# Kernel tuning notes

Hardware: AMD Instinct MI355X
Metric: run time of the kernel (lower is better)

Reference implementation:

```python
import jax, jax.numpy as jnp
import numpy as np

B = 2
D = 256
NH = 8
DH = D // NH
L = 4
K = 2                       # sampling grid per box side
NP = K * K                  # sampled points per level
FF = 1024
NQ = 300
NE = 6
ND = 6
REF_SIZE = 4.0
SHAPES = ((64, 64), (32, 32), (16, 16), (8, 8))
S = sum(h * w for h, w in SHAPES)


def make_ref_windows():
    ws = []
    for (H, W) in SHAPES:
        y = (jnp.arange(1, H + 1, dtype=jnp.float32) - 0.5) / (H + 1e-6)
        x = (jnp.arange(1, W + 1, dtype=jnp.float32) - 0.5) / (W + 1e-6)
        yy, xx = jnp.meshgrid(y, x, indexing='ij')
        ctr = jnp.stack([xx, yy], -1).reshape(-1, 2)
        size = jnp.broadcast_to(jnp.array([REF_SIZE / W, REF_SIZE / H], jnp.float32), ctr.shape)
        ws.append(jnp.concatenate([ctr, size], -1))
    return jnp.broadcast_to(jnp.concatenate(ws, 0)[None], (B, S, 4))


def layernorm(x, g, b):
    m = jnp.mean(x, -1, keepdims=True)
    v = jnp.mean((x - m) ** 2, -1, keepdims=True)
    return (x - m) / jnp.sqrt(v + 1e-5) * g + b


def inverse_sigmoid(x, eps=1e-5):
    x = jnp.clip(x, eps, 1.0 - eps)
    return jnp.log(x / (1.0 - x))


def bilinear_sample(vl, pts, Hl, Wl):
    # vl: [B, Hl*Wl, NH, DH], pts: [B, N, NP, 2] normalized to [0,1]
    x = pts[..., 0] * Wl - 0.5
    y = pts[..., 1] * Hl - 0.5
    x0f = jnp.floor(x); y0f = jnp.floor(y)
    wx = x - x0f; wy = y - y0f
    x0 = x0f.astype(jnp.int32); y0 = y0f.astype(jnp.int32)
    Bn, N, P = x.shape

    def gather(yi, xi):
        valid = ((xi >= 0) & (xi < Wl) & (yi >= 0) & (yi < Hl)).astype(vl.dtype)
        idx = jnp.clip(yi, 0, Hl - 1) * Wl + jnp.clip(xi, 0, Wl - 1)
        g = jnp.take_along_axis(vl, idx.reshape(Bn, N * P, 1, 1), axis=1)
        return g.reshape(Bn, N, P, NH, DH) * valid[..., None, None]

    w00 = ((1 - wx) * (1 - wy))[..., None, None]
    w01 = (wx * (1 - wy))[..., None, None]
    w10 = ((1 - wx) * wy)[..., None, None]
    w11 = (wx * wy)[..., None, None]
    return (gather(y0, x0) * w00 + gather(y0, x0 + 1) * w01
            + gather(y0 + 1, x0) * w10 + gather(y0 + 1, x0 + 1) * w11)


def box_attention(q, memory, ref_windows, Wv, bv, Wa, ba, Wo, bo):
    # q: [B,N,D], memory: [B,S,D], ref_windows: [B,N,4] (cx,cy,w,h)
    Bn, N, _ = q.shape
    v = (memory @ Wv + bv).reshape(Bn, memory.shape[1], NH, DH)
    attn = jax.nn.softmax((q @ Wa + ba).reshape(Bn, N, NH, L * NP), axis=-1)
    g = (jnp.arange(K, dtype=jnp.float32) + 0.5) / K - 0.5   # grid fractions in box
    gy, gx = jnp.meshgrid(g, g, indexing='ij')
    grid = jnp.stack([gx.ravel(), gy.ravel()], -1)           # [NP,2]
    pts = ref_windows[:, :, None, :2] + grid[None, None] * ref_windows[:, :, None, 2:]
    out = jnp.zeros((Bn, N, NH, DH), q.dtype)
    start = 0
    for l, (Hl, Wl) in enumerate(SHAPES):
        sl = Hl * Wl
        sampled = bilinear_sample(v[:, start:start + sl], pts, Hl, Wl)  # [B,N,NP,NH,DH]
        out = out + jnp.einsum('bnphd,bnhp->bnhd', sampled, attn[..., l * NP:(l + 1) * NP])
        start += sl
    return out.reshape(Bn, N, D) @ Wo + bo


def mha(q_in, k_in, v_in, Wqkv, bqkv, Wo, bo):
    Bn, N, _ = q_in.shape
    q = (q_in @ Wqkv[:, :D] + bqkv[:D]).reshape(Bn, N, NH, DH)
    k = (k_in @ Wqkv[:, D:2 * D] + bqkv[D:2 * D]).reshape(Bn, N, NH, DH)
    v = (v_in @ Wqkv[:, 2 * D:] + bqkv[2 * D:]).reshape(Bn, N, NH, DH)
    a = jax.nn.softmax(jnp.einsum('bqhd,bkhd->bhqk', q, k) / jnp.sqrt(jnp.float32(DH)), axis=-1)
    o = jnp.einsum('bhqk,bkhd->bqhd', a, v).reshape(Bn, N, D)
    return o @ Wo + bo


def pos_embed_2d(coords):
    # coords: [B,N,2] -> [B,N,D] sine embedding (deformable-DETR style)
    npf = D // 2
    dim_t = 10000.0 ** (2.0 * (jnp.arange(npf) // 2) / npf)
    p = coords[..., None] * (2 * np.pi) / dim_t               # [B,N,2,npf]
    p = jnp.stack([jnp.sin(p[..., 0::2]), jnp.cos(p[..., 1::2])], -1)
    return p.reshape(coords.shape[0], coords.shape[1], 2 * npf)


def reference(src, pos, eWv, ebv, eWa, eba, eWo, ebo, eW1, eb1, eW2, eb2,
              en1g, en1b, en2g, en2b,
              dWqkv, dbqkv, dWso, dbso, dWv, dbv, dWa, dba, dWo, dbo,
              dW1, db1, dW2, db2, dn1g, dn1b, dn2g, dn2b, dn3g, dn3b,
              cls_w, cls_b, bb_w1, bb_b1, bb_w2, bb_b2, bb_w3, bb_b3,
              el_w, el_b, el_g, el_beta):
    ref_windows = make_ref_windows()
    out = src
    for i in range(NE):
        a = box_attention(out + pos, out, ref_windows, eWv[i], ebv[i], eWa[i], eba[i], eWo[i], ebo[i])
        out = layernorm(out + a, en1g[i], en1b[i])
        f = jax.nn.relu(out @ eW1[i] + eb1[i]) @ eW2[i] + eb2[i]
        out = layernorm(out + f, en2g[i], en2b[i])
    # proposal selection (topk + gather)
    valid = jnp.all((ref_windows[..., :2] > 0.01) & (ref_windows[..., :2] < 0.99), axis=-1)
    logits = (out @ cls_w + cls_b)[..., 0]
    logits = jnp.where(valid, logits, -65504.0)
    _, idx = jax.lax.top_k(logits, NQ)
    q_emb = jnp.take_along_axis(out, idx[..., None], axis=1)
    tgt = layernorm(jax.lax.stop_gradient(q_emb) @ el_w + el_b, el_g, el_beta)
    ref_sel = jnp.take_along_axis(ref_windows, idx[..., None], axis=1)
    h = jax.nn.relu(q_emb @ bb_w1 + bb_b1)
    h = jax.nn.relu(h @ bb_w2 + bb_b2)
    tmp = h @ bb_w3 + bb_b3 + inverse_sigmoid(ref_sel)
    out_ref = jax.lax.stop_gradient(jax.nn.sigmoid(tmp))
    query_pos = pos_embed_2d(out_ref[..., :2]) + pos_embed_2d(out_ref[..., 2:])
    # decoder
    x = tgt
    inter = []
    for i in range(ND):
        qk = x + query_pos
        sa = mha(qk, qk, x, dWqkv[i], dbqkv[i], dWso[i], dbso[i])
        x = layernorm(x + sa, dn1g[i], dn1b[i])
        ca = box_attention(x + query_pos, out, out_ref, dWv[i], dbv[i], dWa[i], dba[i], dWo[i], dbo[i])
        x = layernorm(x + ca, dn2g[i], dn2b[i])
        f = jax.nn.relu(x @ dW1[i] + db1[i]) @ dW2[i] + db2[i]
        x = layernorm(x + f, dn3g[i], dn3b[i])
        inter.append(x)
    return jnp.stack(inter)  # [ND, B, NQ, D]


def setup_inputs() -> dict:
    key = jax.random.key(0)
    kit = iter(jax.random.split(key, 80))
    def rn(shape, s=0.02):
        return jax.random.normal(next(kit), shape, jnp.float32) * s
    z = lambda *sh: jnp.zeros(sh, jnp.float32)
    o = lambda *sh: jnp.ones(sh, jnp.float32)
    A = NH * L * NP
    return dict(
        src=jax.random.normal(next(kit), (B, S, D), jnp.float32),
        pos=jax.random.normal(next(kit), (B, S, D), jnp.float32),
        eWv=rn((NE, D, D)), ebv=z(NE, D), eWa=rn((NE, D, A)), eba=z(NE, A),
        eWo=rn((NE, D, D)), ebo=z(NE, D),
        eW1=rn((NE, D, FF)), eb1=z(NE, FF), eW2=rn((NE, FF, D)), eb2=z(NE, D),
        en1g=o(NE, D), en1b=z(NE, D), en2g=o(NE, D), en2b=z(NE, D),
        dWqkv=rn((ND, D, 3 * D)), dbqkv=z(ND, 3 * D),
        dWso=rn((ND, D, D)), dbso=z(ND, D),
        dWv=rn((ND, D, D)), dbv=z(ND, D), dWa=rn((ND, D, A)), dba=z(ND, A),
        dWo=rn((ND, D, D)), dbo=z(ND, D),
        dW1=rn((ND, D, FF)), db1=z(ND, FF), dW2=rn((ND, FF, D)), db2=z(ND, D),
        dn1g=o(ND, D), dn1b=z(ND, D), dn2g=o(ND, D), dn2b=z(ND, D), dn3g=o(ND, D), dn3b=z(ND, D),
        cls_w=rn((D, 1)), cls_b=z(1),
        bb_w1=rn((D, D)), bb_b1=z(D), bb_w2=rn((D, D)), bb_b2=z(D),
        bb_w3=rn((D, 4)), bb_b3=z(4),
        el_w=rn((D, D)), el_b=z(D), el_g=o(D), el_beta=z(D),
    )
```

## Files before the change

kernel.cpp:

```cpp
#include <hip/hip_runtime.h>
#include <hip/hip_bf16.h>
#include <math.h>

typedef unsigned short u16;
typedef unsigned int u32;
typedef unsigned long long u64;

#define Bc   2
#define NHc  8
#define Sc   5440
#define NQc  300
#define NEc  6
#define NDc  6
#define FFc  1024
#define BSc  (Bc*Sc)
#define BNQc (Bc*NQc)

__device__ __forceinline__ float us2f(u16 u) {
    union { float f; unsigned v; } x; x.v = ((unsigned)u) << 16; return x.f;
}

__device__ __forceinline__ u16 f2bf(float f) {
    unsigned u = __float_as_uint(f);
    unsigned r = u + 0x7FFFu + ((u >> 16) & 1u);
    return (u16)(r >> 16);
}
__device__ __forceinline__ float bf2f(u16 u) { return us2f(u); }
__device__ __forceinline__ unsigned pk2(u16 a, u16 b) { return (unsigned)a | ((unsigned)b << 16); }

__device__ __forceinline__ int xcd_swz(int orig, int nwg) {
    int xcd = orig & 7;
    int q = nwg >> 3, r = nwg & 7;
    int base = (xcd < r) ? xcd * (q + 1) : r * (q + 1) + (xcd - r) * q;
    return base + (orig >> 3);
}

using bf16x8 = __attribute__((ext_vector_type(8))) short;
using f32x4  = __attribute__((ext_vector_type(4))) float;

__global__ void k_detect(const u16* __restrict__ src, int* __restrict__ flag) {
    __shared__ int cnt;
    if (threadIdx.x == 0) cnt = 0;
    __syncthreads();
    u16 v = src[threadIdx.x];
    int e = (v >> 7) & 0xFF;
    int plaus = (e == 0) || (e >= 107 && e <= 131);
    atomicAdd(&cnt, plaus);
    __syncthreads();
    if (threadIdx.x == 0) *flag = (cnt >= 224) ? 1 : 0;
}

struct CvtArgs {
    const void* in[48];
    long off[48];
    int n[48];
    int cnt;
    long total;
};
__global__ void k_cvt_all8(CvtArgs args, float* __restrict__ out,
                           const int* __restrict__ flag) {
    long g = ((long)blockIdx.x * 256 + threadIdx.x) * 8;
    if (g >= args.total) return;
    int lo = 0, hi = args.cnt - 1;
    while (lo < hi) {
        int mid = (lo + hi + 1) >> 1;
        if (args.off[mid] <= g) lo = mid; else hi = mid - 1;
    }
    long local = g - args.off[lo];
    long n = (long)args.n[lo];
    float v[8];
#pragma unroll
    for (int j = 0; j < 8; ++j) v[j] = 0.f;
    if (*flag) {
        const u16* p = (const u16*)args.in[lo] + local;
        if (local + 8 <= n) {
            uint4 r = *(const uint4*)p;
            const u16* pu = (const u16*)&r;
#pragma unroll
            for (int j = 0; j < 8; ++j) v[j] = us2f(pu[j]);
        } else {
            for (int j = 0; j < 8; ++j)
                if (local + j < n) v[j] = us2f(p[j]);
        }
    } else {
        const float* p = (const float*)args.in[lo] + local;
        if (local + 8 <= n) {
            float4 a = ((const float4*)p)[0];
            float4 b = ((const float4*)p)[1];
            v[0] = a.x; v[1] = a.y; v[2] = a.z; v[3] = a.w;
            v[4] = b.x; v[5] = b.y; v[6] = b.z; v[7] = b.w;
        } else {
            for (int j = 0; j < 8; ++j)
                if (local + j < n) v[j] = p[j];
        }
    }
    float4 o0, o1;
    o0.x = v[0]; o0.y = v[1]; o0.z = v[2]; o0.w = v[3];
    o1.x = v[4]; o1.y = v[5]; o1.z = v[6]; o1.w = v[7];
    ((float4*)(out + g))[0] = o0;
    ((float4*)(out + g))[1] = o1;
}

__global__ void k_addf2(const float* __restrict__ a, const float* __restrict__ pos,
                        u16* __restrict__ ah, u16* __restrict__ al,
                        u16* __restrict__ ph, u16* __restrict__ pl, int n) {
    int i = blockIdx.x * 256 + threadIdx.x;
    if (i >= n) return;
    float x = a[i];
    u16 h = f2bf(x);
    ah[i] = h;
    al[i] = f2bf(x - bf2f(h));
    float s = x + pos[i];
    u16 h2 = f2bf(s);
    ph[i] = h2;
    pl[i] = f2bf(s - bf2f(h2));
}

template<int RELU>
__global__ __launch_bounds__(256) void k_mgemm(
    const u16* __restrict__ Ah, const u16* __restrict__ Al,
    const float* __restrict__ W, const u16* __restrict__ Wraw, int ldw,
    const float* __restrict__ bias,
    float* __restrict__ C, u16* __restrict__ Ch, u16* __restrict__ Cl,
    int ldc, int K,
    const int* __restrict__ flag) {
    __shared__ __align__(16) u16 lsAH[4096];
    __shared__ __align__(16) u16 lsAL[4096];
    __shared__ __align__(16) u16 lsBH[4096];
    __shared__ __align__(16) u16 lsBL[4096];
    const int t = threadIdx.x;
    int lin = blockIdx.x + gridDim.x * blockIdx.y;
    lin = xcd_swz(lin, gridDim.x * gridDim.y);
    const int row0 = (lin / gridDim.x) * 128, col0 = (lin % gridDim.x) * 128;
    const int fast = *flag;

    const int c0 = t, c1 = 256 + t;
    const u16* a0h = Ah + (size_t)(row0 + (c0 & 127)) * K + (c0 >> 7) * 8;
    const u16* a1h = Ah + (size_t)(row0 + (c1 & 127)) * K + (c1 >> 7) * 8;
    const u16* a0l = Al + (size_t)(row0 + (c0 & 127)) * K + (c0 >> 7) * 8;
    const u16* a1l = Al + (size_t)(row0 + (c1 & 127)) * K + (c1 >> 7) * 8;

    const int bkp = t >> 4, bno = t & 15;
    const float* bp = W + (size_t)(bkp * 2) * ldw + col0 + bno * 8;
    const u16*  brp = Wraw + (size_t)(bkp * 2) * ldw + col0 + bno * 8;

    const int lane = t & 63;
    const int w = t >> 6;
    const int wr = (w >> 1) * 64, wc = (w & 1) * 64;
    const int kg = lane >> 4, lr = lane & 15;

    f32x4 acc[4][4] = {};
    uint4 aU0h, aU1h, aU0l, aU1l;
    float4 bR[4];
    uint4 bU0, bU1;
    aU0h = *(const uint4*)a0h;
    aU1h = *(const uint4*)a1h;
    aU0l = *(const uint4*)a0l;
    aU1l = *(const uint4*)a1l;
    if (fast) {
        bU0 = *(const uint4*)brp;
        bU1 = *(const uint4*)(brp + ldw);
    } else {
        const float4* q0 = (const float4*)bp;
        const float4* q1 = (const float4*)(bp + ldw);
        bR[0] = q0[0]; bR[1] = q0[1]; bR[2] = q1[0]; bR[3] = q1[1];
    }

    for (int k0 = 0; k0 < K; k0 += 32) {
        if (k0) __syncthreads();
        *(uint4*)&lsAH[(unsigned)c0 * 8u] = aU0h;
        *(uint4*)&lsAH[(unsigned)c1 * 8u] = aU1h;
        *(uint4*)&lsAL[(unsigned)c0 * 8u] = aU0l;
        *(uint4*)&lsAL[(unsigned)c1 * 8u] = aU1l;
        {
            unsigned bb = (unsigned)(bkp >> 2) * 1024u + (unsigned)(bkp & 3) * 2u;
            if (fast) {
                const u16* e0 = (const u16*)&bU0;
                const u16* e1 = (const u16*)&bU1;
#pragma unroll
                for (int j = 0; j < 8; ++j) {
                    int slot = bno * 8 + (j ^ (bno & 7));
                    *(unsigned*)&lsBH[bb + (unsigned)slot * 8u] = pk2(e0[j], e1[j]);
                }
            } else {
                float e0f[8], e1f[8];
                *(float4*)&e0f[0] = bR[0]; *(float4*)&e0f[4] = bR[1];
                *(float4*)&e1f[0] = bR[2]; *(float4*)&e1f[4] = bR[3];
#pragma unroll
                for (int j = 0; j < 8; ++j) {
                    int slot = bno * 8 + (j ^ (bno & 7));
                    u16 h0 = f2bf(e0f[j]), h1 = f2bf(e1f[j]);
                    *(unsigned*)&lsBH[bb + (unsigned)slot * 8u] = pk2(h0, h1);
                    u16 l0 = f2bf(e0f[j] - bf2f(h0));
                    u16 l1 = f2bf(e1f[j] - bf2f(h1));
                    *(unsigned*)&lsBL[bb + (unsigned)slot * 8u] = pk2(l0, l1);
                }
            }
        }
        __syncthreads();
        if (k0 + 32 < K) {
            aU0h = *(const uint4*)(a0h + k0 + 32);
            aU1h = *(const uint4*)(a1h + k0 + 32);
            aU0l = *(const uint4*)(a0l + k0 + 32);
            aU1l = *(const uint4*)(a1l + k0 + 32);
            if (fast) {
                bU0 = *(const uint4*)(brp + (size_t)(k0 + 32) * ldw);
                bU1 = *(const uint4*)(brp + (size_t)(k0 + 33) * ldw);
            } else {
                const float4* q0 = (const float4*)(bp + (size_t)(k0 + 32) * ldw);
                const float4* q1 = (const float4*)(bp + (size_t)(k0 + 33) * ldw);
                bR[0] = q0[0]; bR[1] = q0[1]; bR[2] = q1[0]; bR[3] = q1[1];
            }
        }
        bf16x8 aH[4], aL[4], bH[4], bL[4];
#pragma unroll
        for (int mi = 0; mi < 4; ++mi) {
            unsigned ia = (unsigned)kg * 1024u + (unsigned)(wr + mi * 16 + lr) * 8u;
            aH[mi] = *(const bf16x8*)&lsAH[ia];
            aL[mi] = *(const bf16x8*)&lsAL[ia];
        }
#pragma unroll
        for (int ni = 0; ni < 4; ++ni) {
            int c = wc + ni * 16 + lr;
            int slot = (c & ~7) | ((c ^ (c >> 3)) & 7);
            unsigned ib = (unsigned)kg * 1024u + (unsigned)slot * 8u;
            bH[ni] = *(const bf16x8*)&lsBH[ib];
            if (!fast) bL[ni] = *(const bf16x8*)&lsBL[ib];
        }
#pragma unroll
        for (int mi = 0; mi < 4; ++mi)
#pragma unroll
            for (int ni = 0; ni < 4; ++ni) {
                acc[mi][ni] = __builtin_amdgcn_mfma_f32_16x16x32_bf16(aH[mi], bH[ni], acc[mi][ni], 0, 0, 0);
                acc[mi][ni] = __builtin_amdgcn_mfma_f32_16x16x32_bf16(aL[mi], bH[ni], acc[mi][ni], 0, 0, 0);
            }
        if (!fast) {
#pragma unroll
            for (int mi = 0; mi < 4; ++mi)
#pragma unroll
                for (int ni = 0; ni < 4; ++ni)
                    acc[mi][ni] = __builtin_amdgcn_mfma_f32_16x16x32_bf16(aH[mi], bL[ni], acc[mi][ni], 0, 0, 0);
        }
    }
    const int rb = row0 + wr + (lane >> 4) * 4;
#pragma unroll
    for (int ni = 0; ni < 4; ++ni) {
        int cc = col0 + wc + ni * 16 + lr;
        float bv = bias[cc];
#pragma unroll
        for (int mi = 0; mi < 4; ++mi) {
#pragma unroll
            for (int r2 = 0; r2 < 4; ++r2) {
                int rr = rb + mi * 16 + r2;
                float v = acc[mi][ni][r2] + bv;
                if (RELU) v = fmaxf(v, 0.f);
                size_t ox = (size_t)rr * ldc + cc;
                if (C) C[ox] = v;
                if (Ch) {
                    u16 h = f2bf(v);
                    Ch[ox] = h;
                    Cl[ox] = f2bf(v - bf2f(h));
                }
            }
        }
    }
}

template<int RELU>
__global__ __launch_bounds__(256) void k_dgemm(
    const float* __restrict__ A, int lda,
    const float* __restrict__ W, int ldw, int wcol0,
    const float* __restrict__ bias,
    float* __restrict__ C, int ldc,
    int M, int N, int K) {
    __shared__ float As[2][16][68];
    __shared__ float Bs[2][16][68];
    int t = threadIdx.x;
    int row0 = blockIdx.y * 64, col0 = blockIdx.x * 64;
    int ti = t >> 4, tj = t & 15;
    int arow = t >> 2, akq = (t & 3) << 2;
    int bk = t >> 4, bn = (t & 15) << 2;
    bool aok = (row0 + arow) < M;
    const float* ap = A + (size_t)(row0 + arow) * lda + akq;
    const float* bp = W + (size_t)bk * ldw + wcol0 + col0 + bn;
    float4 aR = aok ? *(const float4*)ap : make_float4(0.f, 0.f, 0.f, 0.f);
    float4 bR = *(const float4*)bp;
    As[0][akq + 0][arow] = aR.x;
    As[0][akq + 1][arow] = aR.y;
    As[0][akq + 2][arow] = aR.z;
    As[0][akq + 3][arow] = aR.w;
    *(float4*)&Bs[0][bk][bn] = bR;
    __syncthreads();
    int cur = 0;
    float acc[4][4] = {};
    for (int k0 = 0; k0 < K; k0 += 16) {
        bool more = (k0 + 16) < K;
        if (more) {
            aR = aok ? *(const float4*)(ap + k0 + 16) : make_float4(0.f, 0.f, 0.f, 0.f);
            bR = *(const float4*)(bp + (size_t)(k0 + 16) * ldw);
        }
#pragma unroll
        for (int k = 0; k < 16; ++k) {
            float a[4], b[4];
#pragma unroll
            for (int r = 0; r < 4; ++r) a[r] = As[cur][k][ti * 4 + r];
#pragma unroll
            for (int c = 0; c < 4; ++c) b[c] = Bs[cur][k][tj * 4 + c];
#pragma unroll
            for (int r = 0; r < 4; ++r)
#pragma unroll
                for (int c = 0; c < 4; ++c) acc[r][c] += a[r] * b[c];
        }
        if (more) {
            int nxt = cur ^ 1;
            As[nxt][akq + 0][arow] = aR.x;
            As[nxt][akq + 1][arow] = aR.y;
            As[nxt][akq + 2][arow] = aR.z;
            As[nxt][akq + 3][arow] = aR.w;
            *(float4*)&Bs[nxt][bk][bn] = bR;
            __syncthreads();
            cur = nxt;
        }
    }
    for (int r = 0; r < 4; ++r) {
        int rr = row0 + ti * 4 + r;
        if (rr >= M) continue;
        for (int c = 0; c < 4; ++c) {
            int cc = col0 + tj * 4 + c;
            float v = acc[r][c] + bias[cc];
            if (RELU) v = fmaxf(v, 0.f);
            C[(size_t)rr * ldc + cc] = v;
        }
    }
}

__global__ __launch_bounds__(256) void k_gemm4(
    const float* __restrict__ A, const float* __restrict__ W,
    const float* __restrict__ bias, const float* __restrict__ rsel,
    float* __restrict__ oref, int M, int K) {
    int row = blockIdx.x * 64 + (threadIdx.x >> 2);
    int col = threadIdx.x & 3;
    if (row >= M) return;
    float acc = 0.f;
    const float* a = A + (size_t)row * K;
    for (int k = 0; k < K; ++k) acc += a[k] * W[k * 4 + col];
    float tmp = acc + bias[col];
    float r = rsel[(size_t)row * 4 + col];
    r = fminf(fmaxf(r, 1e-5f), 1.f - 1e-5f);
    float v = tmp + logf(r / (1.f - r));
    oref[(size_t)row * 4 + col] = 1.f / (1.f + __expf(-v));
}

__global__ void k_ln(const float* __restrict__ a, const float* __restrict__ b,
                     const float* __restrict__ g, const float* __restrict__ be,
                     float* __restrict__ o,
                     u16* __restrict__ oh, u16* __restrict__ ol,
                     const float* __restrict__ padd, float* __restrict__ opadd,
                     u16* __restrict__ oph, u16* __restrict__ opl,
                     void* __restrict__ sdst, size_t soff,
                     const int* __restrict__ flag) {
    int row = blockIdx.x;
    int t = threadIdx.x;
    __shared__ float red[256];
    size_t ix = (size_t)row * 256 + t;
    float x = a[ix];
    if (b) x += b[ix];
    red[t] = x;
    __syncthreads();
    for (int s = 128; s > 0; s >>= 1) { if (t < s) red[t] += red[t + s]; __syncthreads(); }
    float mean = red[0] / 256.f;
    __syncthreads();
    float d = x - mean;
    red[t] = d * d;
    __syncthreads();
    for (int s = 128; s > 0; s >>= 1) { if (t < s) red[t] += red[t + s]; __syncthreads(); }
    float var = red[0] / 256.f;
    float y = d * rsqrtf(var + 1e-5f) * g[t] + be[t];
    o[ix] = y;
    if (oh) {
        u16 h = f2bf(y);
        oh[ix] = h;
        ol[ix] = f2bf(y - bf2f(h));
    }
    if (padd) {
        float z = y + padd[ix];
        if (opadd) opadd[ix] = z;
        if (oph) {
            u16 h = f2bf(z);
            oph[ix] = h;
            opl[ix] = f2bf(z - bf2f(h));
        }
    }
    if (sdst) {
        if (*flag) ((__hip_bfloat16*)sdst)[soff + ix] = __float2bfloat16(y);
        else       ((float*)sdst)[soff + ix] = y;
    }
}

__global__ void k_refw(float* __restrict__ rw) {
    int s = blockIdx.x * 256 + threadIdx.x;
    if (s >= Sc) return;
    int start, HW;
    if (s < 4096)      { start = 0;    HW = 64; }
    else if (s < 5120) { start = 4096; HW = 32; }
    else if (s < 5376) { start = 5120; HW = 16; }
    else               { start = 5376; HW = 8;  }
    int loc = s - start;
    int i = loc / HW, j = loc % HW;
    rw[s * 4 + 0] = (j + 0.5f) / ((float)HW + 1e-6f);
    rw[s * 4 + 1] = (i + 0.5f) / ((float)HW + 1e-6f);
    rw[s * 4 + 2] = 4.0f / (float)HW;
    rw[s * 4 + 3] = 4.0f / (float)HW;
}

__global__ __launch_bounds__(256) void k_box_sample4(
    const float* __restrict__ v, const float* __restrict__ attn,
    const float* __restrict__ refw, int ref_bs,
    float* __restrict__ out, u16* __restrict__ outh, u16* __restrict__ outl,
    int N) {
    const int t = threadIdx.x;
    const int qi = t >> 6, lane = t & 63;
    const int blk = xcd_swz(blockIdx.x, gridDim.x);
    const int n = blk * 4 + qi;
    const int b = blockIdx.y;
    if (n >= N) return;
    const float* arow = attn + ((size_t)b * N + n) * 128;
    float2 wl = *(const float2*)(arow + lane * 2);
    float m = fmaxf(wl.x, wl.y);
#pragma unroll
    for (int d2 = 1; d2 < 8; d2 <<= 1) m = fmaxf(m, __shfl_xor(m, d2, 8));
    float e0 = __expf(wl.x - m), e1 = __expf(wl.y - m);
    float s = e0 + e1;
#pragma unroll
    for (int d2 = 1; d2 < 8; d2 <<= 1) s += __shfl_xor(s, d2, 8);
    float inv = 1.f / s;
    e0 *= inv; e1 *= inv;

    const float* rw = refw + (size_t)ref_bs * b + (size_t)n * 4;
    float cx = rw[0], cy = rw[1], bw = rw[2], bh = rw[3];
    const float* vb = v + (size_t)b * Sc * 256 + lane * 4;
    float4 acc = make_float4(0.f, 0.f, 0.f, 0.f);
    int start = 0;
    const int HWs[4] = {64, 32, 16, 8};
#pragma unroll
    for (int l = 0; l < 4; ++l) {
        int HW = HWs[l];
#pragma unroll
        for (int p = 0; p < 4; ++p) {
            float gx = (p & 1) ? 0.25f : -0.25f;
            float gy = (p >> 1) ? 0.25f : -0.25f;
            float x = (cx + gx * bw) * (float)HW - 0.5f;
            float y = (cy + gy * bh) * (float)HW - 0.5f;
            float x0f = floorf(x), y0f = floorf(y);
            float wx = x - x0f, wy = y - y0f;
            int x0 = (int)x0f, y0 = (int)y0f;
            float4 smp = make_float4(0.f, 0.f, 0.f, 0.f);
            if (x0 >= 0 && x0 < HW && y0 >= 0 && y0 < HW) {
                float4 g4 = *(const float4*)(vb + (size_t)(start + y0 * HW + x0) * 256);
                float wgt = (1.f - wx) * (1.f - wy);
                smp.x += wgt * g4.x; smp.y += wgt * g4.y; smp.z += wgt * g4.z; smp.w += wgt * g4.w;
            }
            if (x0 + 1 >= 0 && x0 + 1 < HW && y0 >= 0 && y0 < HW) {
                float4 g4 = *(const float4*)(vb + (size_t)(start + y0 * HW + x0 + 1) * 256);
                float wgt = wx * (1.f - wy);
                smp.x += wgt * g4.x; smp.y += wgt * g4.y; smp.z += wgt * g4.z; smp.w += wgt * g4.w;
            }
            if (x0 >= 0 && x0 < HW && y0 + 1 >= 0 && y0 + 1 < HW) {
                float4 g4 = *(const float4*)(vb + (size_t)(start + (y0 + 1) * HW + x0) * 256);
                float wgt = (1.f - wx) * wy;
                smp.x += wgt * g4.x; smp.y += wgt * g4.y; smp.z += wgt * g4.z; smp.w += wgt * g4.w;
            }
            if (x0 + 1 >= 0 && x0 + 1 < HW && y0 + 1 >= 0 && y0 + 1 < HW) {
                float4 g4 = *(const float4*)(vb + (size_t)(start + (y0 + 1) * HW + x0 + 1) * 256);
                float wgt = wx * wy;
                smp.x += wgt * g4.x; smp.y += wgt * g4.y; smp.z += wgt * g4.z; smp.w += wgt * g4.w;
            }
            const int idx = l * 4 + p;
            float wsel = (idx & 1) ? e1 : e0;
            float wv = __shfl(wsel, (lane & ~7) | (idx >> 1), 64);
            acc.x += wv * smp.x; acc.y += wv * smp.y;
            acc.z += wv * smp.z; acc.w += wv * smp.w;
        }
        start += HW * HW;
    }
    size_t obase = ((size_t)b * N + n) * 256 + lane * 4;
    if (out) *(float4*)(out + obase) = acc;
    if (outh) {
        ushort4 h, lo;
        h.x = f2bf(acc.x); h.y = f2bf(acc.y); h.z = f2bf(acc.z); h.w = f2bf(acc.w);
        lo.x = f2bf(acc.x - bf2f(h.x)); lo.y = f2bf(acc.y - bf2f(h.y));
        lo.z = f2bf(acc.z - bf2f(h.z)); lo.w = f2bf(acc.w - bf2f(h.w));
        *(ushort4*)(outh + obase) = h;
        *(ushort4*)(outl + obase) = lo;
    }
}

__global__ void k_cls(const float* __restrict__ x, const float* __restrict__ w,
                      const float* __restrict__ cb, const float* __restrict__ rw,
                      float* __restrict__ logits) {
    int row = blockIdx.x;
    int t = threadIdx.x;
    __shared__ float red[256];
    red[t] = x[(size_t)row * 256 + t] * w[t];
    __syncthreads();
    for (int s = 128; s > 0; s >>= 1) { if (t < s) red[t] += red[t + s]; __syncthreads(); }
    if (t == 0) {
        int s = row % Sc;
        float cx = rw[s * 4], cy = rw[s * 4 + 1];
        bool valid = (cx > 0.01f) && (cx < 0.99f) && (cy > 0.01f) && (cy < 0.99f);
        logits[row] = valid ? (red[0] + cb[0]) : -65504.0f;
    }
}

__global__ void k_topk(const float* __restrict__ logits, int* __restrict__ idxout) {
    int b = blockIdx.x;
    int t = threadIdx.x;
    __shared__ unsigned keys[Sc];
    __shared__ int hist[256];
    __shared__ int suf[257];
    __shared__ unsigned sprefix;
    __shared__ int sR;
    __shared__ int cnt;
    __shared__ u64 cand[512];
    for (int i = t; i < Sc; i += 256) {
        union { float f; unsigned u; } x;
        x.f = logits[(size_t)b * Sc + i];
        unsigned u = x.u;
        keys[i] = (u & 0x80000000u) ? ~u : (u | 0x80000000u);
    }
    if (t == 0) { sprefix = 0; sR = NQc; suf[256] = 0; }
    __syncthreads();
    for (int shift = 24; shift >= 0; shift -= 8) {
        hist[t] = 0;
        __syncthreads();
        unsigned pref = sprefix;
        int R = sR;
        unsigned pmask = (shift == 24) ? 0u : (0xFFFFFFFFu << (shift + 8));
        for (int i = t; i < Sc; i += 256) {
            unsigned kk = keys[i];
            if ((kk & pmask) == (pref & pmask))
                atomicAdd(&hist[(kk >> shift) & 255], 1);
        }
        __syncthreads();
        suf[t] = hist[t];
        __syncthreads();
        for (int s2 = 1; s2 < 256; s2 <<= 1) {
            int vv = suf[t] + ((t + s2 < 256) ? suf[t + s2] : 0);
            __syncthreads();
            suf[t] = vv;
            __syncthreads();
        }
        if (suf[t] >= R && suf[t + 1] < R) {
            sR = R - suf[t + 1];
            sprefix = pref | ((unsigned)t << shift);
        }
        __syncthreads();
    }
    unsigned T = sprefix;
    if (t == 0) cnt = 0;
    __syncthreads();
    for (int i = t; i < Sc; i += 256) {
        unsigned kk = keys[i];
        if (kk >= T) {
            int slot = atomicAdd(&cnt, 1);
            if (slot < 512)
                cand[slot] = ~((((u64)kk) << 32) | (u64)(0xFFFFFFFFu - (unsigned)i));
        }
    }
    __syncthreads();
    int total = cnt < 512 ? cnt : 512;
    for (int i = t; i < 512; i += 256)
        if (i >= total) cand[i] = 0xFFFFFFFFFFFFFFFFull;
    __syncthreads();
    for (int i = t; i < 512; i += 256) {
        if (i >= total) continue;
        u64 mine = cand[i];
        int rank = 0;
        for (int j = 0; j < 512; ++j) rank += (cand[j] < mine) ? 1 : 0;
        if (rank < NQc) {
            u64 c = ~mine;
            idxout[b * NQc + rank] = (int)(0xFFFFFFFFu - (unsigned)(c & 0xFFFFFFFFull));
        }
    }
}

__global__ void k_gather(const float* __restrict__ x, const float* __restrict__ rw,
                         const int* __restrict__ idx, float* __restrict__ qemb,
                         float* __restrict__ refsel) {
    int q = blockIdx.x, b = blockIdx.y;
    int t = threadIdx.x;
    int id = idx[b * NQc + q];
    qemb[((size_t)b * NQc + q) * 256 + t] = x[((size_t)b * Sc + id) * 256 + t];
    if (t < 4) refsel[((size_t)b * NQc + q) * 4 + t] = rw[id * 4 + t];
}

__global__ void k_qpos(const float* __restrict__ outref, float* __restrict__ qpos) {
    int n = blockIdx.x, b = blockIdx.y;
    int t = threadIdx.x;
    const float* orf = outref + ((size_t)b * NQc + n) * 4;
    int c = t >> 7;
    int j = (t & 127) >> 1;
    int si = t & 1;
    float tj = powf(10000.f, (float)j / 64.f);
    float sc = 6.283185307179586f / tj;
    float v1 = orf[c] * sc;
    float v2 = orf[2 + c] * sc;
    float r = si ? (cosf(v1) + cosf(v2)) : (sinf(v1) + sinf(v2));
    qpos[((size_t)b * NQc + n) * 256 + t] = r;
}

#define NSPL 10
#define SPLW 30
__global__ __launch_bounds__(256) void k_mha2(
    const float* __restrict__ qk, const float* __restrict__ v,
    float* __restrict__ opart, float* __restrict__ mlpart) {
    __shared__ float lsK[SPLW][256];
    __shared__ float lsV[SPLW][256];
    const int t = threadIdx.x;
    const int h = t >> 5, ql = t & 31;
    const int b = blockIdx.y, z = blockIdx.z;
    const int n = blockIdx.x * 32 + ql;
    const bool qok = n < NQc;
    const int kstart = z * SPLW;
    for (int f = t; f < SPLW * 64; f += 256) {
        int r = f >> 6, c4 = f & 63;
        int krow = kstart + r;
        float4 kv = *(const float4*)(qk + (size_t)(b * NQc + krow) * 512 + 256 + c4 * 4);
        float4 vv = *(const float4*)(v + (size_t)(b * NQc + krow) * 256 + c4 * 4);
        *(float4*)&lsK[r][c4 * 4] = kv;
        *(float4*)&lsV[r][c4 * 4] = vv;
    }
    __syncthreads();
    float q[32];
    {
        const float* qp = qk + (size_t)(b * NQc + (qok ? n : 0)) * 512 + h * 32;
#pragma unroll
        for (int j4 = 0; j4 < 8; ++j4) {
            float4 f = ((const float4*)qp)[j4];
            q[j4 * 4 + 0] = f.x; q[j4 * 4 + 1] = f.y;
            q[j4 * 4 + 2] = f.z; q[j4 * 4 + 3] = f.w;
        }
    }
    const float scale = 0.17677669529663688f;
    float s[SPLW];
#pragma unroll
    for (int kk = 0; kk < SPLW; ++kk) {
        float acc = 0.f;
        const float* kr = &lsK[kk][h * 32];
#pragma unroll
        for (int j4 = 0; j4 < 8; ++j4) {
            float4 kf = ((const float4*)kr)[j4];
            acc += q[j4*4+0]*kf.x + q[j4*4+1]*kf.y + q[j4*4+2]*kf.z + q[j4*4+3]*kf.w;
        }
        s[kk] = acc * scale;
    }
    float m = s[0];
#pragma unroll
    for (int kk = 1; kk < SPLW; ++kk) m = fmaxf(m, s[kk]);
    float o[32];
#pragma unroll
    for (int j = 0; j < 32; ++j) o[j] = 0.f;
    float l = 0.f;
#pragma unroll
    for (int kk = 0; kk < SPLW; ++kk) {
        float e = __expf(s[kk] - m);
        l += e;
        const float* vr = &lsV[kk][h * 32];
#pragma unroll
        for (int j4 = 0; j4 < 8; ++j4) {
            float4 vf = ((const float4*)vr)[j4];
            o[j4*4+0] += e * vf.x; o[j4*4+1] += e * vf.y;
            o[j4*4+2] += e * vf.z; o[j4*4+3] += e * vf.w;
        }
    }
    if (qok) {
        float* op = opart + ((size_t)z * BNQc + (size_t)b * NQc + n) * 256 + h * 32;
#pragma unroll
        for (int j4 = 0; j4 < 8; ++j4) {
            float4 f;
            f.x = o[j4*4+0]; f.y = o[j4*4+1]; f.z = o[j4*4+2]; f.w = o[j4*4+3];
            ((float4*)op)[j4] = f;
        }
        float* mlp = mlpart + ((size_t)z * BNQc + (size_t)b * NQc + n) * 16 + h * 2;
        mlp[0] = m; mlp[1] = l;
    }
}

__global__ void k_mha_comb(const float* __restrict__ opart, const float* __restrict__ mlpart,
                           float* __restrict__ out) {
    int row = blockIdx.x;
    int t = threadIdx.x;
    int h = t >> 5;
    float mm[NSPL], ll[NSPL];
    float M = -3.0e38f;
#pragma unroll
    for (int z = 0; z < NSPL; ++z) {
        mm[z] = mlpart[((size_t)z * BNQc + row) * 16 + h * 2];
        ll[z] = mlpart[((size_t)z * BNQc + row) * 16 + h * 2 + 1];
        M = fmaxf(M, mm[z]);
    }
    float denom = 0.f, osum = 0.f;
#pragma unroll
    for (int z = 0; z < NSPL; ++z) {
        float a = __expf(mm[z] - M);
        denom += ll[z] * a;
        osum += opart[((size_t)z * BNQc + row) * 256 + t] * a;
    }
    out[(size_t)row * 256 + t] = osum / denom;
}

extern "C" void kernel_launch(void* const* d_in, const int* in_sizes, int n_in,
                              void* d_out, int out_size, void* d_ws, size_t ws_size,
                              hipStream_t stream) {
    char* base = (char*)d_ws;
    size_t off = 0;
    auto allocB = [&](size_t bytes) {
        char* p = base + off;
        off = (off + bytes + 255) & ~(size_t)255;
        return p;
    };
    int* flag = (int*)allocB(16);
    auto allocF = [&](size_t n) { return (float*)allocB(n * 4); };
    auto allocH = [&](size_t n) { return (u16*)allocB(n * 2); };

    k_detect<<<1, 256, 0, stream>>>((const u16*)d_in[0], flag);

    CvtArgs ca;
    long acc = 0;
    int ninp = n_in < 48 ? n_in : 48;
    for (int i = 0; i < 48; ++i) {
        int idx2 = i < ninp ? i : ninp - 1;
        ca.in[i] = d_in[idx2];
        ca.n[i] = (i < ninp) ? in_sizes[i] : 0;
        ca.off[i] = acc;
        acc += ((long)ca.n[i] + 63) & ~63L;
    }
    ca.cnt = 48;
    ca.total = acc;
    float* cvtbase = allocF((size_t)acc);
    k_cvt_all8<<<(int)((acc / 8 + 255) / 256), 256, 0, stream>>>(ca, cvtbase, flag);
    float* F[48];
    for (int i = 0; i < 48; ++i) F[i] = cvtbase + ca.off[i];

    const size_t BSD = (size_t)BSc * 256;
    float* enc    = F[0];
    u16* encH  = allocH(BSD);  u16* encL  = allocH(BSD);
    u16* pbufH = allocH(BSD);  u16* pbufL = allocH(BSD);
    u16* tbufH = allocH(BSD);  u16* tbufL = allocH(BSD);
    u16* ffnhH = allocH((size_t)BSc * FFc);
    u16* ffnhL = allocH((size_t)BSc * FFc);
    float* vbuf   = allocF(BSD);
    float* gout   = allocF(BSD);
    float* attnb  = allocF((size_t)BSc * 128);
    float* refw   = allocF(Sc * 4);
    float* logit  = allocF(BSc);
    int*   idx    = (int*)allocB(BNQc * 4);
    float* qemb   = allocF((size_t)BNQc * 256);
    float* rsel   = allocF(BNQc * 4);
    float* xbuf   = allocF((size_t)BNQc * 256);
    float* qposb  = allocF((size_t)BNQc * 256);
    float* dqk    = allocF((size_t)BNQc * 256);
    float* dqk512 = allocF((size_t)BNQc * 512);
    float* dv     = allocF((size_t)BNQc * 256);
    float* dt1    = allocF((size_t)BNQc * 256);
    float* dt2    = allocF((size_t)BNQc * 256);
    float* datt   = allocF((size_t)BNQc * 128);
    float* dffnh  = allocF((size_t)BNQc * FFc);
    float* h1f    = allocF((size_t)BNQc * 256);
    float* h2f    = allocF((size_t)BNQc * 256);
    float* oref   = allocF(BNQc * 4);
    float* opart  = allocF((size_t)NSPL * BNQc * 256);
    float* mlpart = allocF((size_t)NSPL * BNQc * 16);
    (void)ws_size; (void)out_size;

    auto MG = [&](int relu, const u16* Ah, const u16* Al, int widx, size_t woff, int ldw,
                  const float* bias, float* Cf, u16* Ch, u16* Cl, int ldc, int N, int K) {
        const float* Wf = F[widx] + woff;
        const u16* Wraw = (const u16*)d_in[widx] + woff;
        dim3 g(N / 128, BSc / 128);
        if (relu) k_mgemm<1><<<g, 256, 0, stream>>>(Ah, Al, Wf, Wraw, ldw, bias, Cf, Ch, Cl, ldc, K, flag);
        else      k_mgemm<0><<<g, 256, 0, stream>>>(Ah, Al, Wf, Wraw, ldw, bias, Cf, Ch, Cl, ldc, K, flag);
    };
    auto DG = [&](int relu, const float* A, int lda, const float* W, int ldw, int wcol0,
                  const float* bias, float* C, int ldc, int M, int N, int K) {
        dim3 g(N / 64, (M + 63) / 64);
        if (relu) k_dgemm<1><<<g, 256, 0, stream>>>(A, lda, W, ldw, wcol0, bias, C, ldc, M, N, K);
        else      k_dgemm<0><<<g, 256, 0, stream>>>(A, lda, W, ldw, wcol0, bias, C, ldc, M, N, K);
    };

    const int nBSD = (int)BSD;
    k_refw<<<(Sc + 255) / 256, 256, 0, stream>>>(refw);
    k_addf2<<<(nBSD + 255) / 256, 256, 0, stream>>>(enc, F[1], encH, encL, pbufH, pbufL, nBSD);

    for (int i = 0; i < NEc; ++i) {
        MG(0, encH, encL, 2, (size_t)i * 65536, 256, F[3] + i * 256, vbuf, nullptr, nullptr, 256, 256, 256);
        MG(0, pbufH, pbufL, 4, (size_t)i * 32768, 128, F[5] + i * 128, attnb, nullptr, nullptr, 128, 128, 256);
        k_box_sample4<<<dim3((Sc + 3) / 4, Bc), 256, 0, stream>>>(vbuf, attnb, refw, 0,
                                                                  nullptr, tbufH, tbufL, Sc);
        MG(0, tbufH, tbufL, 6, (size_t)i * 65536, 256, F[7] + i * 256, gout, nullptr, nullptr, 256, 256, 256);
        k_ln<<<BSc, 256, 0, stream>>>(enc, gout, F[12] + i * 256, F[13] + i * 256,
                                      enc, encH, encL,
                                      nullptr, nullptr, nullptr, nullptr,
                                      nullptr, 0, flag);
        MG(1, encH, encL, 8, (size_t)i * 262144, 1024, F[9] + i * 1024,
           nullptr, ffnhH, ffnhL, 1024, 1024, 256);
        MG(0, ffnhH, ffnhL, 10, (size_t)i * 262144, 256, F[11] + i * 256,
           gout, nullptr, nullptr, 256, 256, 1024);
        k_ln<<<BSc, 256, 0, stream>>>(enc, gout, F[14] + i * 256, F[15] + i * 256,
                                      enc, encH, encL,
                                      (i < NEc - 1) ? F[1] : nullptr, nullptr,
                                      (i < NEc - 1) ? pbufH : nullptr,
                                      (i < NEc - 1) ? pbufL : nullptr,
                                      nullptr, 0, flag);
    }

    k_cls<<<BSc, 256, 0, stream>>>(enc, F[36], F[37], refw, logit);
    k_topk<<<Bc, 256, 0, stream>>>(logit, idx);
    k_gather<<<dim3(NQc, Bc), 256, 0, stream>>>(enc, refw, idx, qemb, rsel);
    DG(0, qemb, 256, F[44], 256, 0, F[45], dt1, 256, BNQc, 256, 256);
    DG(1, qemb, 256, F[38], 256, 0, F[39], h1f, 256, BNQc, 256, 256);
    DG(1, h1f,  256, F[40], 256, 0, F[41], h2f, 256, BNQc, 256, 256);
    k_gemm4<<<(BNQc + 63) / 64, 256, 0, stream>>>(h2f, F[42], F[43], rsel, oref, BNQc, 256);
    k_qpos<<<dim3(NQc, Bc), 256, 0, stream>>>(oref, qposb);
    k_ln<<<BNQc, 256, 0, stream>>>(dt1, nullptr, F[46], F[47],
                                   xbuf, nullptr, nullptr,
                                   qposb, dqk, nullptr, nullptr,
                                   nullptr, 0, flag);

    const int nXD = BNQc * 256;
    for (int i = 0; i < NDc; ++i) {
        DG(0, dqk,  256, F[16] + (size_t)i * 196608, 768, 0,   F[17] + i * 768,       dqk512, 512, BNQc, 512, 256);
        DG(0, xbuf, 256, F[16] + (size_t)i * 196608, 768, 512, F[17] + i * 768 + 512, dv,     256, BNQc, 256, 256);
        k_mha2<<<dim3((NQc + 31) / 32, Bc, NSPL), 256, 0, stream>>>(dqk512, dv, opart, mlpart);
        k_mha_comb<<<BNQc, 256, 0, stream>>>(opart, mlpart, dt1);
        DG(0, dt1, 256, F[18] + (size_t)i * 65536, 256, 0, F[19] + i * 256, dt2, 256, BNQc, 256, 256);
        k_ln<<<BNQc, 256, 0, stream>>>(xbuf, dt2, F[30] + i * 256, F[31] + i * 256,
                                       xbuf, nullptr, nullptr,
                                       qposb, dqk, nullptr, nullptr,
                                       nullptr, 0, flag);
        MG(0, encH, encL, 20, (size_t)i * 65536, 256, F[21] + i * 256, vbuf, nullptr, nullptr, 256, 256, 256);
        DG(0, dqk, 256, F[22] + (size_t)i * 32768, 128, 0, F[23] + i * 128, datt, 128, BNQc, 128, 256);
        k_box_sample4<<<dim3((NQc + 3) / 4, Bc), 256, 0, stream>>>(vbuf, datt, oref, NQc * 4,
                                                                   dt1, nullptr, nullptr, NQc);
        DG(0, dt1, 256, F[24] + (size_t)i * 65536, 256, 0, F[25] + i * 256, dt2, 256, BNQc, 256, 256);
        k_ln<<<BNQc, 256, 0, stream>>>(xbuf, dt2, F[32] + i * 256, F[33] + i * 256,
                                       xbuf, nullptr, nullptr,
                                       nullptr, nullptr, nullptr, nullptr,
                                       nullptr, 0, flag);
        DG(1, xbuf,  256,  F[26] + (size_t)i * 262144, 1024, 0, F[27] + i * 1024, dffnh, 1024, BNQc, 1024, 256);
        DG(0, dffnh, 1024, F[28] + (size_t)i * 262144, 256,  0, F[29] + i * 256,  dt2,   256,  BNQc, 256, 1024);
        k_ln<<<BNQc, 256, 0, stream>>>(xbuf, dt2, F[34] + i * 256, F[35] + i * 256,
                                       xbuf, nullptr, nullptr,
                                       (i < NDc - 1) ? qposb : nullptr,
                                       (i < NDc - 1) ? dqk : nullptr, nullptr, nullptr,
                                       d_out, (size_t)i * nXD, flag);
    }
}
```

Measured before the change: 2.808 ms.

## Store split-bf16 GEMM activations in K-slab panel layout with swizzled LDS

Changes the hi/lo bf16 activation buffers from row-major to a panel layout of 32-wide K slabs, so each GEMM tile's A load is one contiguous block. All producers (add, layernorm, GEMM epilogue, sampling kernel) write through the new index function. The LDS A tile is also XOR-swizzled on store and fragment read to reduce bank conflicts. Producer stores become strided, and every consumer must agree on the slab stride, which is fixed to the BSc row count.

After: 2.808 ms. Within noise of the previous version (+0.0%).

```diff
diff --git a/kernel.cpp b/kernel.cpp
--- a/kernel.cpp
+++ b/kernel.cpp
@@ -27,6 +27,10 @@
 }
 __device__ __forceinline__ float bf2f(u16 u) { return us2f(u); }
 __device__ __forceinline__ unsigned pk2(u16 a, u16 b) { return (unsigned)a | ((unsigned)b << 16); }
+
+__device__ __forceinline__ size_t pidx(int row, int k) {
+    return (size_t)(k >> 5) * ((size_t)BSc * 32) + ((size_t)row << 5) + (size_t)(k & 31);
+}
 
 __device__ __forceinline__ int xcd_swz(int orig, int nwg) {
     int xcd = orig & 7;
@@ -106,14 +110,16 @@
                         u16* __restrict__ ph, u16* __restrict__ pl, int n) {
     int i = blockIdx.x * 256 + threadIdx.x;
     if (i >= n) return;
+    int row = i >> 8, k = i & 255;
+    size_t px = pidx(row, k);
     float x = a[i];
     u16 h = f2bf(x);
-    ah[i] = h;
-    al[i] = f2bf(x - bf2f(h));
+    ah[px] = h;
+    al[px] = f2bf(x - bf2f(h));
     float s = x + pos[i];
     u16 h2 = f2bf(s);
-    ph[i] = h2;
-    pl[i] = f2bf(s - bf2f(h2));
+    ph[px] = h2;
+    pl[px] = f2bf(s - bf2f(h2));
 }
 
 template<int RELU>
@@ -133,12 +139,16 @@
     lin = xcd_swz(lin, gridDim.x * gridDim.y);
     const int row0 = (lin / gridDim.x) * 128, col0 = (lin % gridDim.x) * 128;
     const int fast = *flag;
+    const size_t PSLAB = (size_t)BSc * 32;
 
     const int c0 = t, c1 = 256 + t;
-    const u16* a0h = Ah + (size_t)(row0 + (c0 & 127)) * K + (c0 >> 7) * 8;
-    const u16* a1h = Ah + (size_t)(row0 + (c1 & 127)) * K + (c1 >> 7) * 8;
-    const u16* a0l = Al + (size_t)(row0 + (c0 & 127)) * K + (c0 >> 7) * 8;
-    const u16* a1l = Al + (size_t)(row0 + (c1 & 127)) * K + (c1 >> 7) * 8;
+    const size_t abase = (size_t)row0 * 32;
+    const u16* a0h = Ah + abase + (size_t)c0 * 8;
+    const u16* a1h = Ah + abase + (size_t)c1 * 8;
+    const u16* a0l = Al + abase + (size_t)c0 * 8;
+    const u16* a1l = Al + abase + (size_t)c1 * 8;
+    const unsigned d0 = (((unsigned)c0 & ~3u) | (((unsigned)c0 & 3u) ^ (((unsigned)c0 >> 3) & 3u))) * 8u;
+    const unsigned d1 = (((unsigned)c1 & ~3u) | (((unsigned)c1 & 3u) ^ (((unsigned)c1 >> 3) & 3u))) * 8u;
 
     const int bkp = t >> 4, bno = t & 15;
     const float* bp = W + (size_t)(bkp * 2) * ldw + col0 + bno * 8;
@@ -148,6 +158,13 @@
     const int w = t >> 6;
     const int wr = (w >> 1) * 64, wc = (w & 1) * 64;
     const int kg = lane >> 4, lr = lane & 15;
+
+    unsigned iaf[4];
+#pragma unroll
+    for (int mi = 0; mi < 4; ++mi) {
+        int arow = wr + mi * 16 + lr;
+        iaf[mi] = ((unsigned)(arow << 2) + ((unsigned)kg ^ (((unsigned)arow >> 1) & 3u))) * 8u;
+    }
 
     f32x4 acc[4][4] = {};
     uint4 aU0h, aU1h, aU0l, aU1l;
@@ -168,10 +185,10 @@
 
     for (int k0 = 0; k0 < K; k0 += 32) {
         if (k0) __syncthreads();
-        *(uint4*)&lsAH[(unsigned)c0 * 8u] = aU0h;
-        *(uint4*)&lsAH[(unsigned)c1 * 8u] = aU1h;
-        *(uint4*)&lsAL[(unsigned)c0 * 8u] = aU0l;
-        *(uint4*)&lsAL[(unsigned)c1 * 8u] = aU1l;
+        *(uint4*)&lsAH[d0] = aU0h;
+        *(uint4*)&lsAH[d1] = aU1h;
+        *(uint4*)&lsAL[d0] = aU0l;
+        *(uint4*)&lsAL[d1] = aU1l;
         {
             unsigned bb = (unsigned)(bkp >> 2) * 1024u + (unsigned)(bkp & 3) * 2u;
             if (fast) {
@@ -199,10 +216,11 @@
         }
         __syncthreads();
         if (k0 + 32 < K) {
-            aU0h = *(const uint4*)(a0h + k0 + 32);
-            aU1h = *(const uint4*)(a1h + k0 + 32);
-            aU0l = *(const uint4*)(a0l + k0 + 32);
-            aU1l = *(const uint4*)(a1l + k0 + 32);
+            size_t soff = (size_t)((k0 >> 5) + 1) * PSLAB;
+            aU0h = *(const uint4*)(a0h + soff);
+            aU1h = *(const uint4*)(a1h + soff);
+            aU0l = *(const uint4*)(a0l + soff);
+            aU1l = *(const uint4*)(a1l + soff);
             if (fast) {
                 bU0 = *(const uint4*)(brp + (size_t)(k0 + 32) * ldw);
                 bU1 = *(const uint4*)(brp + (size_t)(k0 + 33) * ldw);
@@ -215,9 +233,8 @@
         bf16x8 aH[4], aL[4], bH[4], bL[4];
 #pragma unroll
         for (int mi = 0; mi < 4; ++mi) {
-            unsigned ia = (unsigned)kg * 1024u + (unsigned)(wr + mi * 16 + lr) * 8u;
-            aH[mi] = *(const bf16x8*)&lsAH[ia];
-            aL[mi] = *(const bf16x8*)&lsAL[ia];
+            aH[mi] = *(const bf16x8*)&lsAH[iaf[mi]];
+            aL[mi] = *(const bf16x8*)&lsAL[iaf[mi]];
         }
 #pragma unroll
         for (int ni = 0; ni < 4; ++ni) {
@@ -254,12 +271,12 @@
                 int rr = rb + mi * 16 + r2;
                 float v = acc[mi][ni][r2] + bv;
                 if (RELU) v = fmaxf(v, 0.f);
-                size_t ox = (size_t)rr * ldc + cc;
-                if (C) C[ox] = v;
+                if (C) C[(size_t)rr * ldc + cc] = v;
                 if (Ch) {
+                    size_t px = pidx(rr, cc);
                     u16 h = f2bf(v);
-                    Ch[ox] = h;
-                    Cl[ox] = f2bf(v - bf2f(h));
+                    Ch[px] = h;
+                    Cl[px] = f2bf(v - bf2f(h));
                 }
             }
         }
@@ -378,17 +395,19 @@
     float y = d * rsqrtf(var + 1e-5f) * g[t] + be[t];
     o[ix] = y;
     if (oh) {
+        size_t px = pidx(row, t);
         u16 h = f2bf(y);
-        oh[ix] = h;
-        ol[ix] = f2bf(y - bf2f(h));
+        oh[px] = h;
+        ol[px] = f2bf(y - bf2f(h));
     }
     if (padd) {
         float z = y + padd[ix];
         if (opadd) opadd[ix] = z;
         if (oph) {
+            size_t px = pidx(row, t);
             u16 h = f2bf(z);
-            oph[ix] = h;
-            opl[ix] = f2bf(z - bf2f(h));
+            oph[px] = h;
+            opl[px] = f2bf(z - bf2f(h));
         }
     }
     if (sdst) {
@@ -483,15 +502,18 @@
         }
         start += HW * HW;
     }
-    size_t obase = ((size_t)b * N + n) * 256 + lane * 4;
-    if (out) *(float4*)(out + obase) = acc;
+    if (out) {
+        size_t obase = ((size_t)b * N + n) * 256 + lane * 4;
+        *(float4*)(out + obase) = acc;
+    }
     if (outh) {
+        size_t px = pidx(b * N + n, lane * 4);
         ushort4 h, lo;
         h.x = f2bf(acc.x); h.y = f2bf(acc.y); h.z = f2bf(acc.z); h.w = f2bf(acc.w);
         lo.x = f2bf(acc.x - bf2f(h.x)); lo.y = f2bf(acc.y - bf2f(h.y));
         lo.z = f2bf(acc.z - bf2f(h.z)); lo.w = f2bf(acc.w - bf2f(h.w));
-        *(ushort4*)(outh + obase) = h;
-        *(ushort4*)(outl + obase) = lo;
+        *(ushort4*)(outh + px) = h;
+        *(ushort4*)(outl + px) = lo;
     }
 }
 
```
